# Kernel tuning notes

Hardware: AMD Instinct MI355X
Metric: run time of the kernel (lower is better)

The kernel has to match this reference:

```python
import jax, jax.numpy as jnp
import numpy as np

N, T, H, D = 8, 192, 1024, 128
P = 4            # t_patch_size (kernel = stride)
TP = T // P      # 48 patch tokens
E = 16384
HOUR, WDAY = 48, 7


def conv1d_patch(e, W, b):
    # e: [B, Cin, T]; W: [Cout, Cin, P]; kernel == stride == P (non-overlapping)
    B, Ci, Tt = e.shape
    e = e.reshape(B, Ci, Tt // P, P)
    return jnp.einsum('bctk,ock->bot', e, W) + b[None, :, None]  # [B, Cout, T']


def gcn_propagate(x, src, dst, coef):
    # x: [B, H, D] ; symmetric-normalized sparse A_hat @ x
    msg = x[:, src, :] * coef[None, :, None]
    return jnp.zeros_like(x).at[:, dst, :].add(msg)


def setup_inputs() -> dict:
    key = jax.random.key(0)
    ks = jax.random.split(key, 12)
    x = jax.random.normal(ks[0], (N, 1, T, H, 1), dtype=jnp.float32)
    x_mark = jax.random.randint(ks[1], (N, T, 2), 0, 7).astype(jnp.int64)
    edges = jax.random.randint(ks[2], (E, 2), 0, H).astype(jnp.int64)
    node_split = jnp.arange(H, dtype=jnp.int64).reshape(4, 256)
    s = 0.02
    params = {
        'hour_emb': jax.random.normal(ks[3], (HOUR, D), jnp.float32) * s,
        'weekday_emb': jax.random.normal(ks[4], (WDAY, D), jnp.float32) * s,
        'timeconv_w': jax.random.normal(ks[5], (D, D, P), jnp.float32) * s,
        'timeconv_b': jnp.zeros((D,), jnp.float32),
        'tconv_w': jax.random.normal(ks[6], (D, 1, P), jnp.float32) * s,
        'tconv_b': jnp.zeros((D,), jnp.float32),
        'W1': jax.random.normal(ks[7], (D, D), jnp.float32) * s,
        'b1': jnp.zeros((D,), jnp.float32),
        'W2': jax.random.normal(ks[8], (D, D), jnp.float32) * s,
        'b2': jnp.zeros((D,), jnp.float32),
    }
    return dict(x=x, x_mark=x_mark, edges=edges, node_split=node_split, **params)


def reference(x, x_mark, edges, node_split, hour_emb, weekday_emb,
              timeconv_w, timeconv_b, tconv_w, tconv_b, W1, b1, W2, b2):
    # ---- TimeEmb (TemporalEmbedding, hour_num='48') ----
    hour_x = hour_emb[x_mark[:, :, 1]]        # [N, T, D]
    wday_x = weekday_emb[x_mark[:, :, 0]]     # [N, T, D]
    time_emb = conv1d_patch((hour_x + wday_x).transpose(0, 2, 1),
                            timeconv_w, timeconv_b).transpose(0, 2, 1)  # [N, T', D]

    # ---- temporal value embedding ----
    xv = jnp.squeeze(x, (1, 4)).transpose(0, 2, 1).reshape(N * H, 1, T)  # [N*H,1,T]
    tv = conv1d_patch(xv, tconv_w, tconv_b)                 # [N*H, D, T']
    tv = tv.transpose(0, 2, 1).reshape(N, H, TP, D)         # [N, H, T', D]
    tv = tv.transpose(0, 2, 1, 3).reshape(N * TP, H, D)     # [N*T', H, D]

    # ---- 2-layer GCN with self-loops + symmetric normalization ----
    src = jnp.concatenate([edges[:, 0], jnp.arange(H)])
    dst = jnp.concatenate([edges[:, 1], jnp.arange(H)])
    deg = jnp.zeros((H,), tv.dtype).at[dst].add(1.0)
    coef = jax.lax.rsqrt(deg[src] * deg[dst])
    h = jax.nn.relu(gcn_propagate(tv, src, dst, coef) @ W1 + b1)
    token = gcn_propagate(h, src, dst, coef) @ W2 + b2      # [N*T', H, D]
    token = token.reshape(N, TP, H, D)

    # ---- per-group gather + mean pooling, interleaved per time step ----
    G = node_split.shape[0]
    grouped = token[:, :, node_split.reshape(-1), :].reshape(N, TP, G, -1, D)
    token = grouped.mean(axis=3).reshape(N, TP * G, D)      # [N, T'*G, D]

    time_rep = jnp.repeat(time_emb, G, axis=1)              # [N, T'*G, D]
    out = token + time_rep  # is_time == 1; eval mode -> no dropout
    return out, time_rep
```

## Files before the change

kernel.cpp:

```cpp
#include <hip/hip_runtime.h>
#include <hip/hip_bf16.h>

#define NN 8
#define TT 192
#define HH 1024
#define DD 128
#define TPP 48
#define EE 16384
#define NEDGE (EE + HH)
#define BB (NN * TPP)
#define NOUT (NN * TT * DD)

typedef short bf16x8 __attribute__((ext_vector_type(8)));
typedef float f32x4 __attribute__((ext_vector_type(4)));

__device__ __forceinline__ float us2f(unsigned short u) {
  union { unsigned i; float f; } t;
  t.i = ((unsigned)u) << 16;
  return t.f;
}

__device__ __forceinline__ void acc6(float cf, unsigned u0, unsigned u1, unsigned u2,
                                     float& a0, float& a1, float& a2, float& a3,
                                     float& a4, float& a5) {
  union { unsigned i; float f; } lo, hi;
  lo.i = u0 << 16; hi.i = u0 & 0xffff0000u;
  a0 = fmaf(cf, lo.f, a0); a1 = fmaf(cf, hi.f, a1);
  lo.i = u1 << 16; hi.i = u1 & 0xffff0000u;
  a2 = fmaf(cf, lo.f, a2); a3 = fmaf(cf, hi.f, a3);
  lo.i = u2 << 16; hi.i = u2 & 0xffff0000u;
  a4 = fmaf(cf, lo.f, a4); a5 = fmaf(cf, hi.f, a5);
}

__global__ __launch_bounds__(256) void k_setup(
    const int* __restrict__ edges, const int* __restrict__ node_split,
    const float* __restrict__ x, __hip_bfloat16* __restrict__ Xall,
    const float* __restrict__ tcw, const float* __restrict__ tcb,
    const float* __restrict__ W1, float* __restrict__ CW,
    const float* __restrict__ W2, __hip_bfloat16* __restrict__ w2sw,
    int* __restrict__ fill, int* __restrict__ csr_src, float* __restrict__ csr_coef,
    float* __restrict__ csum, float* __restrict__ QT, int* __restrict__ row_ptr,
    const int* __restrict__ xm, const float* __restrict__ hour_emb,
    const float* __restrict__ wday_emb, const float* __restrict__ tw,
    float* __restrict__ out) {
  __shared__ float tile[64][65];
  __shared__ int hist[1024];
  __shared__ int rp2[1024];
  __shared__ int invS[1024];
  __shared__ int wsumS[4];
  int tid = threadIdx.x, bid = blockIdx.x;
  if (bid < 384) {
    int tt = bid % 24, st = bid / 24;
    int t0 = tt * 64, s0 = st * 64;
    int sl = tid & 63, r4 = tid >> 6;
#pragma unroll 4
    for (int ii = 0; ii < 16; ++ii) {
      int tl = ii * 4 + r4;
      tile[tl][sl] = x[(size_t)(t0 + tl) * HH + s0 + sl];
    }
    __syncthreads();
#pragma unroll 4
    for (int ii = 0; ii < 16; ++ii) {
      int sl2 = ii * 4 + r4;
      Xall[(size_t)(s0 + sl2) * 1536 + t0 + sl] = __float2bfloat16(tile[sl][sl2]);
    }
  } else if (bid < 452) {
    int ex = (bid - 384) * 256 + tid;
    if (ex < 640) {
      int j = ex >> 7, o = ex & 127;
      float acc = 0.f;
      if (j < 4)
        for (int d = 0; d < DD; ++d) acc = fmaf(tcw[d * 4 + j], W1[d * DD + o], acc);
      else
        for (int d = 0; d < DD; ++d) acc = fmaf(tcb[d], W1[d * DD + o], acc);
      CW[j * DD + o] = acc;
    }
    int ew = ex - 1024;
    if (ew >= 0 && ew < 16384) {
      int n = ew >> 7, k = ew & 127;
      int dstb = n * 256 + (((k >> 3) ^ (n & 7)) * 16) + (k & 7) * 2;
      w2sw[dstb >> 1] = __float2bfloat16(W2[k * DD + n]);
    }
  } else if (bid < 520) {
    int lane = tid & 63, wid = tid >> 6;
    for (int i = tid; i < 1024; i += 256) hist[i] = 1;
    for (int i = tid; i < 1024; i += 256) invS[node_split[i]] = i;
    __syncthreads();
    for (int e = tid; e < EE; e += 256) atomicAdd(&hist[edges[2 * e + 1]], 1);
    __syncthreads();
    int4 d4 = ((const int4*)hist)[tid];
    int l0 = d4.x, l1 = d4.y, l2 = d4.z, l3 = d4.w;
    int lsum = l0 + l1 + l2 + l3;
    int incl = lsum;
#pragma unroll
    for (int off = 1; off < 64; off <<= 1) {
      int u = __shfl_up(incl, off, 64);
      if (lane >= off) incl += u;
    }
    if (lane == 63) wsumS[wid] = incl;
    __syncthreads();
    int base = 0;
    if (wid > 0) base += wsumS[0];
    if (wid > 1) base += wsumS[1];
    if (wid > 2) base += wsumS[2];
    int excl = base + incl - lsum;
    rp2[4 * tid] = excl;
    rp2[4 * tid + 1] = excl + l0;
    rp2[4 * tid + 2] = excl + l0 + l1;
    rp2[4 * tid + 3] = excl + l0 + l1 + l2;
    __syncthreads();
    if (bid == 452) {
      for (int i = tid; i < 1024; i += 256) row_ptr[i] = rp2[i];
      if (tid == 0) row_ptr[1024] = NEDGE;
    }
    int e = (bid - 452) * 256 + tid;
    int s, dt;
    if (e < EE) {
      int2 ed = ((const int2*)edges)[e];
      s = ed.x; dt = ed.y;
    } else {
      s = dt = e - EE;
    }
    float cf = rsqrtf((float)hist[s] * (float)hist[dt]);
    int pos = atomicAdd(&fill[dt], 1);
    int at = rp2[dt] + pos;
    csr_src[at] = s;
    csr_coef[at] = cf;
    atomicAdd(&csum[dt], cf);
    int g = invS[dt] >> 8;
    atomicAdd(&QT[s * 4 + g], cf * (1.0f / 256.0f));
  } else {
    __shared__ float sL[2][512];
    int bb = bid - 520;
    int half = tid >> 7, o = tid & 127;
    int b = bb * 2 + half;
    int n = b / TPP, tp = b % TPP;
    for (int k = 0; k < 4; ++k) {
      int t = tp * 4 + k;
      int wd = xm[(n * TT + t) * 2 + 0];
      int hr = xm[(n * TT + t) * 2 + 1];
      sL[half][o * 4 + k] = hour_emb[hr * DD + o] + wday_emb[wd * DD + o];
    }
    __syncthreads();
    const float* twr = tw + (size_t)o * 512;
    float a0 = tcb[o], a1 = 0.f, a2 = 0.f, a3 = 0.f;
    for (int j = 0; j < 512; j += 4) {
      a0 = fmaf(sL[half][j + 0], twr[j + 0], a0);
      a1 = fmaf(sL[half][j + 1], twr[j + 1], a1);
      a2 = fmaf(sL[half][j + 2], twr[j + 2], a2);
      a3 = fmaf(sL[half][j + 3], twr[j + 3], a3);
    }
    float acc = (a0 + a1) + (a2 + a3);
    size_t base = (size_t)NOUT + ((size_t)n * TT + tp * 4) * DD + o;
    out[base] = acc;
    out[base + DD] = acc;
    out[base + 2 * DD] = acc;
    out[base + 3 * DD] = acc;
  }
}

__global__ __launch_bounds__(256) void k_spmm(
    const int* __restrict__ row_ptr, const int* __restrict__ csr_src,
    const float* __restrict__ csr_coef, const __hip_bfloat16* __restrict__ Xall,
    __hip_bfloat16* __restrict__ xbar) {
  __shared__ int sS[256];
  __shared__ float sC[256];
  int tid = threadIdx.x, h = blockIdx.x;
  int j0 = row_ptr[h], j1 = row_ptr[h + 1];
  int cnt = j1 - j0;
  int cs = cnt < 256 ? cnt : 256;
  if (tid < cs) { sS[tid] = csr_src[j0 + tid]; sC[tid] = csr_coef[j0 + tid]; }
  __syncthreads();
  float a0 = 0.f, a1 = 0.f, a2 = 0.f, a3 = 0.f, a4 = 0.f, a5 = 0.f;
  int j = 0;
  for (; j + 4 <= cs; j += 4) {
    const unsigned* x0 = (const unsigned*)(Xall + (size_t)sS[j] * 1536);
    const unsigned* x1 = (const unsigned*)(Xall + (size_t)sS[j + 1] * 1536);
    const unsigned* x2 = (const unsigned*)(Xall + (size_t)sS[j + 2] * 1536);
    const unsigned* x3 = (const unsigned*)(Xall + (size_t)sS[j + 3] * 1536);
    unsigned u00 = x0[tid], u01 = x0[tid + 256], u02 = x0[tid + 512];
    unsigned u10 = x1[tid], u11 = x1[tid + 256], u12 = x1[tid + 512];
    unsigned u20 = x2[tid], u21 = x2[tid + 256], u22 = x2[tid + 512];
    unsigned u30 = x3[tid], u31 = x3[tid + 256], u32 = x3[tid + 512];
    float c0 = sC[j], c1 = sC[j + 1], c2 = sC[j + 2], c3 = sC[j + 3];
    acc6(c0, u00, u01, u02, a0, a1, a2, a3, a4, a5);
    acc6(c1, u10, u11, u12, a0, a1, a2, a3, a4, a5);
    acc6(c2, u20, u21, u22, a0, a1, a2, a3, a4, a5);
    acc6(c3, u30, u31, u32, a0, a1, a2, a3, a4, a5);
  }
  for (; j < cs; ++j) {
    const unsigned* xr = (const unsigned*)(Xall + (size_t)sS[j] * 1536);
    unsigned u0 = xr[tid], u1 = xr[tid + 256], u2 = xr[tid + 512];
    acc6(sC[j], u0, u1, u2, a0, a1, a2, a3, a4, a5);
  }
  for (; j < cnt; ++j) {
    int s = csr_src[j0 + j];
    float cf = csr_coef[j0 + j];
    const unsigned* xr = (const unsigned*)(Xall + (size_t)s * 1536);
    unsigned u0 = xr[tid], u1 = xr[tid + 256], u2 = xr[tid + 512];
    acc6(cf, u0, u1, u2, a0, a1, a2, a3, a4, a5);
  }
  unsigned* xw = (unsigned*)(xbar + (size_t)h * 1536);
  union { __hip_bfloat16 h2[2]; unsigned u; } pk;
  pk.h2[0] = __float2bfloat16(a0); pk.h2[1] = __float2bfloat16(a1);
  xw[tid] = pk.u;
  pk.h2[0] = __float2bfloat16(a2); pk.h2[1] = __float2bfloat16(a3);
  xw[tid + 256] = pk.u;
  pk.h2[0] = __float2bfloat16(a4); pk.h2[1] = __float2bfloat16(a5);
  xw[tid + 512] = pk.u;
}

__global__ __launch_bounds__(128) void k_red(const __hip_bfloat16* __restrict__ xbar,
                                             const float* __restrict__ csum,
                                             const float* __restrict__ QT,
                                             const float* __restrict__ CW,
                                             const float* __restrict__ b1,
                                             float* __restrict__ ypar) {
  __shared__ float4 xb4[256];
  __shared__ float4 qv[256];
  __shared__ float csv[256];
  __shared__ float yL[512];
  int tid = threadIdx.x, bid = blockIdx.x;
  int b = bid >> 2, qt = bid & 3;
  for (int r = tid; r < 256; r += 128) {
    int h = qt * 256 + r;
    ushort4 us = *(const ushort4*)(xbar + (size_t)h * 1536 + b * 4);
    xb4[r] = make_float4(us2f(us.x), us2f(us.y), us2f(us.z), us2f(us.w));
    qv[r] = *(const float4*)(QT + h * 4);
    csv[r] = csum[h];
  }
  int lane = tid & 63, w = tid >> 6;
  int o0 = lane, o1 = lane + 64;
  float cw0a = CW[o0], cw1a = CW[DD + o0], cw2a = CW[2 * DD + o0];
  float cw3a = CW[3 * DD + o0], cw4a = CW[4 * DD + o0];
  float cw0b = CW[o1], cw1b = CW[DD + o1], cw2b = CW[2 * DD + o1];
  float cw3b = CW[3 * DD + o1], cw4b = CW[4 * DD + o1];
  float b1a = b1[o0], b1b = b1[o1];
  __syncthreads();
  float y0a = 0.f, y1a = 0.f, y2a = 0.f, y3a = 0.f;
  float y0b = 0.f, y1b = 0.f, y2b = 0.f, y3b = 0.f;
  int h0 = w * 128;
#pragma unroll 4
  for (int hh = h0; hh < h0 + 128; ++hh) {
    float4 xv = xb4[hh];
    float4 q = qv[hh];
    float c = csv[hh];
    float t0 = fmaf(c, cw4a, b1a);
    t0 = fmaf(xv.x, cw0a, t0);
    t0 = fmaf(xv.y, cw1a, t0);
    t0 = fmaf(xv.z, cw2a, t0);
    t0 = fmaf(xv.w, cw3a, t0);
    t0 = fmaxf(t0, 0.f);
    float t1 = fmaf(c, cw4b, b1b);
    t1 = fmaf(xv.x, cw0b, t1);
    t1 = fmaf(xv.y, cw1b, t1);
    t1 = fmaf(xv.z, cw2b, t1);
    t1 = fmaf(xv.w, cw3b, t1);
    t1 = fmaxf(t1, 0.f);
    y0a = fmaf(q.x, t0, y0a); y1a = fmaf(q.y, t0, y1a);
    y2a = fmaf(q.z, t0, y2a); y3a = fmaf(q.w, t0, y3a);
    y0b = fmaf(q.x, t1, y0b); y1b = fmaf(q.y, t1, y1b);
    y2b = fmaf(q.z, t1, y2b); y3b = fmaf(q.w, t1, y3b);
  }
  if (w == 0) {
    yL[o0] = y0a; yL[128 + o0] = y1a; yL[256 + o0] = y2a; yL[384 + o0] = y3a;
    yL[o1] = y0b; yL[128 + o1] = y1b; yL[256 + o1] = y2b; yL[384 + o1] = y3b;
  }
  __syncthreads();
  if (w == 1) {
    yL[o0] += y0a; yL[128 + o0] += y1a; yL[256 + o0] += y2a; yL[384 + o0] += y3a;
    yL[o1] += y0b; yL[128 + o1] += y1b; yL[256 + o1] += y2b; yL[384 + o1] += y3b;
  }
  __syncthreads();
  float* yp = ypar + ((size_t)qt * BB + b) * 512;
  for (int i = tid; i < 512; i += 128) yp[i] = yL[i];
}

__global__ __launch_bounds__(256, 2) void k_out(const float* __restrict__ ypar,
                                                const __hip_bfloat16* __restrict__ w2sw,
                                                const float* __restrict__ b2,
                                                float* __restrict__ out) {
  __shared__ __align__(16) char Wr[32768];
  __shared__ __align__(16) char Gr[16384];
  int tid = threadIdx.x;
  int m0 = blockIdx.x * 64;
  {
    const uint4* ws = (const uint4*)w2sw;
    uint4* wd = (uint4*)Wr;
    for (int i = tid; i < 2048; i += 256) wd[i] = ws[i];
  }
#pragma unroll 4
  for (int it = 0; it < 16; ++it) {
    int pi = it * 256 + tid;
    int row = pi >> 6, kp = pi & 63;
    int base = (m0 + row) * 128 + 2 * kp;
    float s0 = 0.f, s1 = 0.f;
#pragma unroll
    for (int p = 0; p < 4; ++p) {
      s0 += ypar[(size_t)p * (BB * 512) + base];
      s1 += ypar[(size_t)p * (BB * 512) + base + 1];
    }
    union { __hip_bfloat16 h[2]; unsigned u; } pk;
    pk.h[0] = __float2bfloat16(s0);
    pk.h[1] = __float2bfloat16(s1);
    *(unsigned*)(Gr + row * 256 + (((kp >> 2) ^ (row & 7)) * 16) + (kp & 3) * 4) = pk.u;
  }
  int lane = tid & 63, w = tid >> 6;
  int colq = lane & 15, quad = lane >> 4;
  float bo[8];
#pragma unroll
  for (int jn = 0; jn < 8; ++jn) bo[jn] = b2[jn * 16 + colq];
  __syncthreads();

  f32x4 acc[8];
#pragma unroll
  for (int jn = 0; jn < 8; ++jn) acc[jn] = (f32x4){0.f, 0.f, 0.f, 0.f};
  int arow = w * 16 + colq;
#pragma unroll
  for (int kc = 0; kc < 4; ++kc) {
    bf16x8 af = *(const bf16x8*)(Gr + arow * 256 + (((kc * 4 + quad) ^ (arow & 7)) * 16));
#pragma unroll
    for (int jn = 0; jn < 8; ++jn) {
      int nr = jn * 16 + colq;
      bf16x8 bf = *(const bf16x8*)(Wr + nr * 256 + (((kc * 4 + quad) ^ (nr & 7)) * 16));
      acc[jn] = __builtin_amdgcn_mfma_f32_16x16x32_bf16(af, bf, acc[jn], 0, 0, 0);
    }
  }
#pragma unroll
  for (int reg = 0; reg < 4; ++reg) {
    int m = m0 + w * 16 + quad * 4 + reg;
    int b = m >> 2, g = m & 3;
    int n_ = b / TPP, tp = b % TPP;
    size_t rb = ((size_t)(n_ * TT + tp * 4 + g)) * DD;
#pragma unroll
    for (int jn = 0; jn < 8; ++jn) {
      int o = jn * 16 + colq;
      out[rb + o] = acc[jn][reg] + bo[jn] + out[(size_t)NOUT + rb + o];
    }
  }
}

extern "C" void kernel_launch(void* const* d_in, const int* in_sizes, int n_in,
                              void* d_out, int out_size, void* d_ws, size_t ws_size,
                              hipStream_t stream) {
  const float* x = (const float*)d_in[0];
  const int* xm = (const int*)d_in[1];
  const int* edges = (const int*)d_in[2];
  const int* node_split = (const int*)d_in[3];
  const float* hour_emb = (const float*)d_in[4];
  const float* wday_emb = (const float*)d_in[5];
  const float* timeconv_w = (const float*)d_in[6];
  const float* timeconv_b = (const float*)d_in[7];
  const float* tcw = (const float*)d_in[8];
  const float* tcb = (const float*)d_in[9];
  const float* W1 = (const float*)d_in[10];
  const float* b1 = (const float*)d_in[11];
  const float* W2 = (const float*)d_in[12];
  const float* b2 = (const float*)d_in[13];
  float* out = (float*)d_out;

  char* w = (char*)d_ws;
  int* fill = (int*)(w + 4096);
  float* csum = (float*)(w + 8192);
  float* QT = (float*)(w + 12288);
  int* row_ptr = (int*)(w + 28672);
  int* csr_src = (int*)(w + 37120);
  float* csr_coef = (float*)(w + 106752);
  __hip_bfloat16* w2sw = (__hip_bfloat16*)(w + 176384);
  float* CW = (float*)(w + 209152);
  __hip_bfloat16* Xall = (__hip_bfloat16*)(w + 475392);
  float* ypar = (float*)(w + 475392);
  __hip_bfloat16* xbar = (__hip_bfloat16*)(w + 3621120);

  hipMemsetAsync(w + 4096, 0, 24576, stream);
  k_setup<<<712, 256, 0, stream>>>(edges, node_split, x, Xall, tcw, tcb, W1, CW, W2,
                                   w2sw, fill, csr_src, csr_coef, csum, QT, row_ptr,
                                   xm, hour_emb, wday_emb, timeconv_w, out);
  k_spmm<<<HH, 256, 0, stream>>>(row_ptr, csr_src, csr_coef, Xall, xbar);
  k_red<<<BB * 4, 128, 0, stream>>>(xbar, csum, QT, CW, b1, ypar);
  k_out<<<24, 256, 0, stream>>>(ypar, w2sw, b2, out);
}
```

Baseline: 141.3 us.

## Precompute per-tap embedding-conv tables and spread time embedding across kernels

The time-embedding conv is rewritten using linearity. Hour and weekday embeddings are each projected once through the conv weights, giving 48x4 and 7x4 lookup tables built in extra k_spmm blocks from a transposed weight copy made in k_setup. The output time_rep is then produced in extra k_red blocks by summing table lookups, replacing the 512-length dot product per output. To host those blocks, k_red is widened to 256 threads with half the threads idle on the main path, which costs occupancy and adds dummy barriers.

```diff
diff --git a/kernel.cpp b/kernel.cpp
--- a/kernel.cpp
+++ b/kernel.cpp
@@ -40,9 +40,7 @@
     const float* __restrict__ W2, __hip_bfloat16* __restrict__ w2sw,
     int* __restrict__ fill, int* __restrict__ csr_src, float* __restrict__ csr_coef,
     float* __restrict__ csum, float* __restrict__ QT, int* __restrict__ row_ptr,
-    const int* __restrict__ xm, const float* __restrict__ hour_emb,
-    const float* __restrict__ wday_emb, const float* __restrict__ tw,
-    float* __restrict__ out) {
+    const float* __restrict__ tw, float* __restrict__ twT) {
   __shared__ float tile[64][65];
   __shared__ int hist[1024];
   __shared__ int rp2[1024];
@@ -50,6 +48,8 @@
   __shared__ int wsumS[4];
   int tid = threadIdx.x, bid = blockIdx.x;
   if (bid < 384) {
+    int i = bid * 256 + tid;
+    if (i < 65536) twT[(i & 511) * DD + (i >> 9)] = tw[i];
     int tt = bid % 24, st = bid / 24;
     int t0 = tt * 64, s0 = st * 64;
     int sl = tid & 63, r4 = tid >> 6;
@@ -81,7 +81,7 @@
       int dstb = n * 256 + (((k >> 3) ^ (n & 7)) * 16) + (k & 7) * 2;
       w2sw[dstb >> 1] = __float2bfloat16(W2[k * DD + n]);
     }
-  } else if (bid < 520) {
+  } else {
     int lane = tid & 63, wid = tid >> 6;
     for (int i = tid; i < 1024; i += 256) hist[i] = 1;
     for (int i = tid; i < 1024; i += 256) invS[node_split[i]] = i;
@@ -129,43 +129,39 @@
     atomicAdd(&csum[dt], cf);
     int g = invS[dt] >> 8;
     atomicAdd(&QT[s * 4 + g], cf * (1.0f / 256.0f));
-  } else {
-    __shared__ float sL[2][512];
-    int bb = bid - 520;
-    int half = tid >> 7, o = tid & 127;
-    int b = bb * 2 + half;
-    int n = b / TPP, tp = b % TPP;
-    for (int k = 0; k < 4; ++k) {
-      int t = tp * 4 + k;
-      int wd = xm[(n * TT + t) * 2 + 0];
-      int hr = xm[(n * TT + t) * 2 + 1];
-      sL[half][o * 4 + k] = hour_emb[hr * DD + o] + wday_emb[wd * DD + o];
-    }
-    __syncthreads();
-    const float* twr = tw + (size_t)o * 512;
-    float a0 = tcb[o], a1 = 0.f, a2 = 0.f, a3 = 0.f;
-    for (int j = 0; j < 512; j += 4) {
-      a0 = fmaf(sL[half][j + 0], twr[j + 0], a0);
-      a1 = fmaf(sL[half][j + 1], twr[j + 1], a1);
-      a2 = fmaf(sL[half][j + 2], twr[j + 2], a2);
-      a3 = fmaf(sL[half][j + 3], twr[j + 3], a3);
-    }
-    float acc = (a0 + a1) + (a2 + a3);
-    size_t base = (size_t)NOUT + ((size_t)n * TT + tp * 4) * DD + o;
-    out[base] = acc;
-    out[base + DD] = acc;
-    out[base + 2 * DD] = acc;
-    out[base + 3 * DD] = acc;
   }
 }
 
 __global__ __launch_bounds__(256) void k_spmm(
     const int* __restrict__ row_ptr, const int* __restrict__ csr_src,
     const float* __restrict__ csr_coef, const __hip_bfloat16* __restrict__ Xall,
-    __hip_bfloat16* __restrict__ xbar) {
+    __hip_bfloat16* __restrict__ xbar, const float* __restrict__ twT,
+    const float* __restrict__ hour_emb, const float* __restrict__ wday_emb,
+    float* __restrict__ UV) {
   __shared__ int sS[256];
   __shared__ float sC[256];
-  int tid = threadIdx.x, h = blockIdx.x;
+  int tid = threadIdx.x, bid = blockIdx.x;
+  if (bid >= HH) {
+    int i = (bid - HH) * 256 + tid;
+    if (i < 24576) {
+      int o = i & 127, r = i >> 7;
+      int hr = r % 48, k = r / 48;
+      float acc = 0.f;
+      for (int d = 0; d < DD; ++d)
+        acc = fmaf(twT[(d * 4 + k) * DD + o], hour_emb[hr * DD + d], acc);
+      UV[i] = acc;
+    } else if (i < 28160) {
+      int j = i - 24576;
+      int o = j & 127, r = j >> 7;
+      int wd = r % 7, k = r / 7;
+      float acc = 0.f;
+      for (int d = 0; d < DD; ++d)
+        acc = fmaf(twT[(d * 4 + k) * DD + o], wday_emb[wd * DD + d], acc);
+      UV[i] = acc;
+    }
+    return;
+  }
+  int h = bid;
   int j0 = row_ptr[h], j1 = row_ptr[h + 1];
   int cnt = j1 - j0;
   int cs = cnt < 256 ? cnt : 256;
@@ -210,70 +206,104 @@
   xw[tid + 512] = pk.u;
 }
 
-__global__ __launch_bounds__(128) void k_red(const __hip_bfloat16* __restrict__ xbar,
+__global__ __launch_bounds__(256) void k_red(const __hip_bfloat16* __restrict__ xbar,
                                              const float* __restrict__ csum,
                                              const float* __restrict__ QT,
                                              const float* __restrict__ CW,
                                              const float* __restrict__ b1,
-                                             float* __restrict__ ypar) {
+                                             float* __restrict__ ypar,
+                                             const int* __restrict__ xm,
+                                             const float* __restrict__ tcb,
+                                             const float* __restrict__ UV,
+                                             float* __restrict__ out) {
   __shared__ float4 xb4[256];
   __shared__ float4 qv[256];
   __shared__ float csv[256];
   __shared__ float yL[512];
   int tid = threadIdx.x, bid = blockIdx.x;
+  if (bid >= 1536) {
+    int bb = bid - 1536;
+    int half = tid >> 7, o = tid & 127;
+    int b = bb * 2 + half;
+    int n = b / TPP, tp = b % TPP;
+    const float* U = UV;
+    const float* V = UV + 24576;
+    float acc = tcb[o];
+#pragma unroll
+    for (int k = 0; k < 4; ++k) {
+      int t = tp * 4 + k;
+      int wd = xm[(n * TT + t) * 2 + 0];
+      int hr = xm[(n * TT + t) * 2 + 1];
+      acc += U[k * 6144 + hr * DD + o] + V[k * 896 + wd * DD + o];
+    }
+    size_t base = (size_t)NOUT + ((size_t)n * TT + tp * 4) * DD + o;
+    out[base] = acc;
+    out[base + DD] = acc;
+    out[base + 2 * DD] = acc;
+    out[base + 3 * DD] = acc;
+    return;
+  }
   int b = bid >> 2, qt = bid & 3;
-  for (int r = tid; r < 256; r += 128) {
-    int h = qt * 256 + r;
-    ushort4 us = *(const ushort4*)(xbar + (size_t)h * 1536 + b * 4);
-    xb4[r] = make_float4(us2f(us.x), us2f(us.y), us2f(us.z), us2f(us.w));
-    qv[r] = *(const float4*)(QT + h * 4);
-    csv[r] = csum[h];
+  if (tid < 128) {
+    for (int r = tid; r < 256; r += 128) {
+      int h = qt * 256 + r;
+      ushort4 us = *(const ushort4*)(xbar + (size_t)h * 1536 + b * 4);
+      xb4[r] = make_float4(us2f(us.x), us2f(us.y), us2f(us.z), us2f(us.w));
+      qv[r] = *(const float4*)(QT + h * 4);
+      csv[r] = csum[h];
+    }
   }
   int lane = tid & 63, w = tid >> 6;
-  int o0 = lane, o1 = lane + 64;
-  float cw0a = CW[o0], cw1a = CW[DD + o0], cw2a = CW[2 * DD + o0];
-  float cw3a = CW[3 * DD + o0], cw4a = CW[4 * DD + o0];
-  float cw0b = CW[o1], cw1b = CW[DD + o1], cw2b = CW[2 * DD + o1];
-  float cw3b = CW[3 * DD + o1], cw4b = CW[4 * DD + o1];
-  float b1a = b1[o0], b1b = b1[o1];
-  __syncthreads();
-  float y0a = 0.f, y1a = 0.f, y2a = 0.f, y3a = 0.f;
-  float y0b = 0.f, y1b = 0.f, y2b = 0.f, y3b = 0.f;
-  int h0 = w * 128;
+  if (tid < 128) {
+    int o0 = lane, o1 = lane + 64;
+    float cw0a = CW[o0], cw1a = CW[DD + o0], cw2a = CW[2 * DD + o0];
+    float cw3a = CW[3 * DD + o0], cw4a = CW[4 * DD + o0];
+    float cw0b = CW[o1], cw1b = CW[DD + o1], cw2b = CW[2 * DD + o1];
+    float cw3b = CW[3 * DD + o1], cw4b = CW[4 * DD + o1];
+    float b1a = b1[o0], b1b = b1[o1];
+    __syncthreads();
+    float y0a = 0.f, y1a = 0.f, y2a = 0.f, y3a = 0.f;
+    float y0b = 0.f, y1b = 0.f, y2b = 0.f, y3b = 0.f;
+    int h0 = w * 128;
 #pragma unroll 4
-  for (int hh = h0; hh < h0 + 128; ++hh) {
-    float4 xv = xb4[hh];
-    float4 q = qv[hh];
-    float c = csv[hh];
-    float t0 = fmaf(c, cw4a, b1a);
-    t0 = fmaf(xv.x, cw0a, t0);
-    t0 = fmaf(xv.y, cw1a, t0);
-    t0 = fmaf(xv.z, cw2a, t0);
-    t0 = fmaf(xv.w, cw3a, t0);
-    t0 = fmaxf(t0, 0.f);
-    float t1 = fmaf(c, cw4b, b1b);
-    t1 = fmaf(xv.x, cw0b, t1);
-    t1 = fmaf(xv.y, cw1b, t1);
-    t1 = fmaf(xv.z, cw2b, t1);
-    t1 = fmaf(xv.w, cw3b, t1);
-    t1 = fmaxf(t1, 0.f);
-    y0a = fmaf(q.x, t0, y0a); y1a = fmaf(q.y, t0, y1a);
-    y2a = fmaf(q.z, t0, y2a); y3a = fmaf(q.w, t0, y3a);
-    y0b = fmaf(q.x, t1, y0b); y1b = fmaf(q.y, t1, y1b);
-    y2b = fmaf(q.z, t1, y2b); y3b = fmaf(q.w, t1, y3b);
-  }
-  if (w == 0) {
-    yL[o0] = y0a; yL[128 + o0] = y1a; yL[256 + o0] = y2a; yL[384 + o0] = y3a;
-    yL[o1] = y0b; yL[128 + o1] = y1b; yL[256 + o1] = y2b; yL[384 + o1] = y3b;
-  }
-  __syncthreads();
-  if (w == 1) {
-    yL[o0] += y0a; yL[128 + o0] += y1a; yL[256 + o0] += y2a; yL[384 + o0] += y3a;
-    yL[o1] += y0b; yL[128 + o1] += y1b; yL[256 + o1] += y2b; yL[384 + o1] += y3b;
-  }
-  __syncthreads();
-  float* yp = ypar + ((size_t)qt * BB + b) * 512;
-  for (int i = tid; i < 512; i += 128) yp[i] = yL[i];
+    for (int hh = h0; hh < h0 + 128; ++hh) {
+      float4 xv = xb4[hh];
+      float4 q = qv[hh];
+      float c = csv[hh];
+      float t0 = fmaf(c, cw4a, b1a);
+      t0 = fmaf(xv.x, cw0a, t0);
+      t0 = fmaf(xv.y, cw1a, t0);
+      t0 = fmaf(xv.z, cw2a, t0);
+      t0 = fmaf(xv.w, cw3a, t0);
+      t0 = fmaxf(t0, 0.f);
+      float t1 = fmaf(c, cw4b, b1b);
+      t1 = fmaf(xv.x, cw0b, t1);
+      t1 = fmaf(xv.y, cw1b, t1);
+      t1 = fmaf(xv.z, cw2b, t1);
+      t1 = fmaf(xv.w, cw3b, t1);
+      t1 = fmaxf(t1, 0.f);
+      y0a = fmaf(q.x, t0, y0a); y1a = fmaf(q.y, t0, y1a);
+      y2a = fmaf(q.z, t0, y2a); y3a = fmaf(q.w, t0, y3a);
+      y0b = fmaf(q.x, t1, y0b); y1b = fmaf(q.y, t1, y1b);
+      y2b = fmaf(q.z, t1, y2b); y3b = fmaf(q.w, t1, y3b);
+    }
+    if (w == 0) {
+      yL[o0] = y0a; yL[128 + o0] = y1a; yL[256 + o0] = y2a; yL[384 + o0] = y3a;
+      yL[o1] = y0b; yL[128 + o1] = y1b; yL[256 + o1] = y2b; yL[384 + o1] = y3b;
+    }
+    __syncthreads();
+    if (w == 1) {
+      yL[o0] += y0a; yL[128 + o0] += y1a; yL[256 + o0] += y2a; yL[384 + o0] += y3a;
+      yL[o1] += y0b; yL[128 + o1] += y1b; yL[256 + o1] += y2b; yL[384 + o1] += y3b;
+    }
+    __syncthreads();
+    float* yp = ypar + ((size_t)qt * BB + b) * 512;
+    for (int i = tid; i < 512; i += 128) yp[i] = yL[i];
+  } else {
+    __syncthreads();
+    __syncthreads();
+    __syncthreads();
+  }
 }
 
 __global__ __launch_bounds__(256, 2) void k_out(const float* __restrict__ ypar,
@@ -368,15 +398,19 @@
   float* csr_coef = (float*)(w + 106752);
   __hip_bfloat16* w2sw = (__hip_bfloat16*)(w + 176384);
   float* CW = (float*)(w + 209152);
+  float* twT = (float*)(w + 213248);
   __hip_bfloat16* Xall = (__hip_bfloat16*)(w + 475392);
   float* ypar = (float*)(w + 475392);
   __hip_bfloat16* xbar = (__hip_bfloat16*)(w + 3621120);
+  float* UV = (float*)(w + 6766848);
 
   hipMemsetAsync(w + 4096, 0, 24576, stream);
-  k_setup<<<712, 256, 0, stream>>>(edges, node_split, x, Xall, tcw, tcb, W1, CW, W2,
+  k_setup<<<520, 256, 0, stream>>>(edges, node_split, x, Xall, tcw, tcb, W1, CW, W2,
                                    w2sw, fill, csr_src, csr_coef, csum, QT, row_ptr,
-                                   xm, hour_emb, wday_emb, timeconv_w, out);
-  k_spmm<<<HH, 256, 0, stream>>>(row_ptr, csr_src, csr_coef, Xall, xbar);
-  k_red<<<BB * 4, 128, 0, stream>>>(xbar, csum, QT, CW, b1, ypar);
+                                   timeconv_w, twT);
+  k_spmm<<<HH + 110, 256, 0, stream>>>(row_ptr, csr_src, csr_coef, Xall, xbar, twT,
+                                       hour_emb, wday_emb, UV);
+  k_red<<<1536 + 192, 256, 0, stream>>>(xbar, csum, QT, CW, b1, ypar, xm, tcb, UV,
+                                        out);
   k_out<<<24, 256, 0, stream>>>(ypar, w2sw, b2, out);
 }
```

Result: slower. 145.3 us (+2.8%).
